# Performance work log

Measured on AMD Instinct MI355X. Metric: run time of the kernel, lower is better.

## Reference

```python
import jax, jax.numpy as jnp
import numpy as np

IMG = 800          # image size (square)
STRIDE = 4         # feature-map stride
S = 14             # rcnn_crop_size
C = 256            # crop_channels
N = 512            # number of rpn proposals
NUM_CLASSES = 81   # COCO (incl. background at index 0)
HID = 1024
NMS_TH = 0.5
SCORE_TH = 0.05


def setup_inputs() -> dict:
    key = jax.random.key(0)
    ks = jax.random.split(key, 8)
    features = jax.random.normal(ks[0], (1, C, IMG // STRIDE, IMG // STRIDE), jnp.float32)
    # valid proposal boxes (x0, y0, x1, y1) in image coordinates
    u = jax.random.uniform(ks[1], (N, 4), jnp.float32)
    x0 = u[:, 0] * (IMG - 64.0)
    y0 = u[:, 1] * (IMG - 64.0)
    bw = 16.0 + u[:, 2] * 240.0
    bh = 16.0 + u[:, 3] * 240.0
    proposals = jnp.stack([x0, y0, jnp.minimum(x0 + bw, IMG - 1.0), jnp.minimum(y0 + bh, IMG - 1.0)], axis=1)
    d1 = C * S * S  # 50176
    w1 = jax.random.normal(ks[2], (d1, HID), jnp.float32) * (1.0 / np.sqrt(d1))
    b1 = jnp.zeros((HID,), jnp.float32)
    w2 = jax.random.normal(ks[3], (HID, HID), jnp.float32) * (1.0 / np.sqrt(HID))
    b2 = jnp.zeros((HID,), jnp.float32)
    w_cls = jax.random.normal(ks[4], (HID, NUM_CLASSES), jnp.float32) * (1.0 / np.sqrt(HID))
    b_cls = jnp.zeros((NUM_CLASSES,), jnp.float32)
    w_reg = jax.random.normal(ks[5], (HID, NUM_CLASSES * 4), jnp.float32) * (1.0 / np.sqrt(HID))
    b_reg = jnp.zeros((NUM_CLASSES * 4,), jnp.float32)
    return dict(features=features, proposals=proposals, w1=w1, b1=b1, w2=w2, b2=b2,
                w_cls=w_cls, b_cls=b_cls, w_reg=w_reg, b_reg=b_reg)


def roi_align(feat, boxes):
    """feat: [C,H,W]; boxes: [N,4] image coords -> crops [N,C,S,S] via bilinear sampling (1 sample per bin)."""
    _, H, W = feat.shape
    b = boxes / STRIDE
    t = (jnp.arange(S, dtype=feat.dtype) + 0.5) / S                # [S] bin centers
    xs = b[:, 0:1] + (b[:, 2:3] - b[:, 0:1]) * t                   # [N,S]
    ys = b[:, 1:2] + (b[:, 3:4] - b[:, 1:2]) * t                   # [N,S]
    xx = jnp.broadcast_to(xs[:, None, :], (boxes.shape[0], S, S))  # [N,S,S]
    yy = jnp.broadcast_to(ys[:, :, None], (boxes.shape[0], S, S))
    x0f = jnp.floor(xx); y0f = jnp.floor(yy)
    fx = xx - x0f; fy = yy - y0f
    x0i = jnp.clip(x0f.astype(jnp.int32), 0, W - 1); x1i = jnp.clip(x0i + 1, 0, W - 1)
    y0i = jnp.clip(y0f.astype(jnp.int32), 0, H - 1); y1i = jnp.clip(y0i + 1, 0, H - 1)
    # gathers -> [C,N,S,S]
    v = (((1 - fx) * (1 - fy))[None] * feat[:, y0i, x0i]
         + (fx * (1 - fy))[None] * feat[:, y0i, x1i]
         + ((1 - fx) * fy)[None] * feat[:, y1i, x0i]
         + (fx * fy)[None] * feat[:, y1i, x1i])
    return v.transpose(1, 0, 2, 3)  # [N,C,S,S]


def decode_boxes(rois, d):
    w = rois[:, 2] - rois[:, 0]; h = rois[:, 3] - rois[:, 1]
    cx = rois[:, 0] + 0.5 * w; cy = rois[:, 1] + 0.5 * h
    px = cx + d[:, 0] * w; py = cy + d[:, 1] * h
    pw = w * jnp.exp(jnp.clip(d[:, 2], -4.0, 4.0))
    ph = h * jnp.exp(jnp.clip(d[:, 3], -4.0, 4.0))
    b = jnp.stack([px - 0.5 * pw, py - 0.5 * ph, px + 0.5 * pw, py + 0.5 * ph], axis=1)
    return jnp.clip(b, 0.0, IMG - 1.0)


def iou_matrix(b):
    area = jnp.maximum(b[:, 2] - b[:, 0], 0.0) * jnp.maximum(b[:, 3] - b[:, 1], 0.0)
    ix0 = jnp.maximum(b[:, None, 0], b[None, :, 0])
    iy0 = jnp.maximum(b[:, None, 1], b[None, :, 1])
    ix1 = jnp.minimum(b[:, None, 2], b[None, :, 2])
    iy1 = jnp.minimum(b[:, None, 3], b[None, :, 3])
    inter = jnp.maximum(ix1 - ix0, 0.0) * jnp.maximum(iy1 - iy0, 0.0)
    return inter / (area[:, None] + area[None, :] - inter + 1e-6)


def reference(features, proposals, w1, b1, w2, b2, w_cls, b_cls, w_reg, b_reg):
    # 1) RoIAlign crop
    crops = roi_align(features[0], proposals)              # [N,C,S,S]
    # 2) RCNN head
    x = crops.reshape(N, -1)
    x = jax.nn.relu(x @ w1 + b1)
    x = jax.nn.relu(x @ w2 + b2)
    logits = x @ w_cls + b_cls                             # [N,81]
    deltas = (x @ w_reg + b_reg).reshape(N, NUM_CLASSES, 4)
    # 3) NMS post-processing
    probs = jax.nn.softmax(logits, axis=-1)
    fg = probs[:, 1:]                                      # exclude background
    labels = jnp.argmax(fg, axis=-1) + 1                   # [N]
    scores = jnp.max(fg, axis=-1)                          # [N]
    d = deltas[jnp.arange(N), labels]                      # per-ROI delta of predicted class
    boxes = decode_boxes(proposals, d)
    order = jnp.argsort(-scores)
    bs = boxes[order]; ss = scores[order]; ls = labels[order]
    valid = ss > SCORE_TH
    M = iou_matrix(bs)                                     # [N,N]
    idx = jnp.arange(N)
    def body(i, keep):
        alive = keep[i] & valid[i]
        supp = (M[i] > NMS_TH) & (idx > i) & alive
        return keep & (~supp)
    keep = jax.lax.fori_loop(0, N, body, valid)
    keepf = jax.lax.stop_gradient(keep.astype(bs.dtype))
    final = jnp.concatenate([bs, ss[:, None]], axis=1) * keepf[:, None]   # [N,5]
    return final, ls.astype(jnp.int32), keep
```

## Files before the change

kernel.cpp:

```cpp
#include <hip/hip_runtime.h>
#include <cstdint>

#define F_H 200
#define F_W 200
#define D1  50176
#define NBOX 512
#define NHID 1024

typedef _Float16 f16;
typedef _Float16 half8 __attribute__((ext_vector_type(8)));
typedef float    f32x4 __attribute__((ext_vector_type(4)));

__device__ __forceinline__ void gload16(const void* g, void* l) {
  __builtin_amdgcn_global_load_lds((const __attribute__((address_space(1))) void*)g,
                                   (__attribute__((address_space(3))) void*)l,
                                   16, 0, 0);
}

__device__ __forceinline__ void splitf16(float v, f16& h, f16& l) {
  f16 hh = (f16)v;
  float hf = (float)hh;
  if (fabsf(hf) < 6.1035156e-5f) hf = 0.f;
  h = (f16)hf;
  l = (f16)((v - hf) * 2048.f);
}

__global__ __launch_bounds__(256) void k_roi(const float* __restrict__ feat,
                                             const float* __restrict__ prop,
                                             f16* __restrict__ xhi, f16* __restrict__ xlo) {
  uint32_t idx = blockIdx.x * 256u + threadIdx.x;
  uint32_t n = idx / D1;
  uint32_t rem = idx % D1;
  uint32_t c = rem / 196u;
  uint32_t r2 = rem % 196u;
  uint32_t i = r2 / 14u;
  uint32_t j = r2 % 14u;
  float b0 = prop[n * 4 + 0] * 0.25f, b1 = prop[n * 4 + 1] * 0.25f;
  float b2 = prop[n * 4 + 2] * 0.25f, b3 = prop[n * 4 + 3] * 0.25f;
  float tx = ((float)j + 0.5f) * (1.0f / 14.0f);
  float ty = ((float)i + 0.5f) * (1.0f / 14.0f);
  float xx = b0 + (b2 - b0) * tx;
  float yy = b1 + (b3 - b1) * ty;
  float x0f = floorf(xx), y0f = floorf(yy);
  float fx = xx - x0f, fy = yy - y0f;
  int x0 = (int)x0f; x0 = x0 < 0 ? 0 : (x0 > F_W - 1 ? F_W - 1 : x0);
  int y0 = (int)y0f; y0 = y0 < 0 ? 0 : (y0 > F_H - 1 ? F_H - 1 : y0);
  int x1 = x0 + 1 > F_W - 1 ? F_W - 1 : x0 + 1;
  int y1 = y0 + 1 > F_H - 1 ? F_H - 1 : y0 + 1;
  const float* fc = feat + (size_t)c * (F_H * F_W);
  float v00 = fc[y0 * F_W + x0], v01 = fc[y0 * F_W + x1];
  float v10 = fc[y1 * F_W + x0], v11 = fc[y1 * F_W + x1];
  float v = (1.f - fx) * (1.f - fy) * v00 + fx * (1.f - fy) * v01 +
            (1.f - fx) * fy * v10 + fx * fy * v11;
  f16 h, l; splitf16(v, h, l);
  xhi[idx] = h; xlo[idx] = l;
}

__global__ __launch_bounds__(256) void k_pack(const float* __restrict__ wc, const float* __restrict__ bc,
                                              const float* __restrict__ wr, const float* __restrict__ br,
                                              float* __restrict__ wh, float* __restrict__ bh) {
  uint32_t idx = blockIdx.x * 256u + threadIdx.x;
  if (idx < (uint32_t)NHID * 512u) {
    uint32_t k = idx >> 9, n = idx & 511u;
    float v = 0.f;
    if (n < 81u) v = wc[k * 81u + n];
    else if (n < 405u) v = wr[k * 324u + (n - 81u)];
    wh[idx] = v;
  } else if (idx < (uint32_t)NHID * 512u + 512u) {
    uint32_t n = idx - (uint32_t)NHID * 512u;
    float v = 0.f;
    if (n < 81u) v = bc[n];
    else if (n < 405u) v = br[n - 81u];
    bh[n] = v;
  }
}

__global__ __launch_bounds__(512, 2) void k_gemm(
    const f16* __restrict__ Ahi, const f16* __restrict__ Alo,
    const float* __restrict__ B, float* __restrict__ Cp,
    int K, int N, int Kc, int nMt, int nNt)
{
  __shared__ char sm[131072];
  const int t = threadIdx.x;
  const int lane = t & 63;
  const int wid = t >> 6;
  const int wr = wid >> 2;
  const int wc = wid & 3;
  const int rl = lane & 15;
  const int lq = lane >> 4;

  int bid = blockIdx.x;
  int low = bid & 7, q = bid >> 3;
  int nt = q % nNt;
  int chi = q / nNt;
  int c = chi * 8 + low;
  int ks = c / nMt;
  int mt = c % nMt;
  const int brow = mt * 256;
  const int nbase = nt * 256;
  const int k0 = ks * Kc;
  const int nk = Kc >> 5;

  uint32_t aoffg[2], aldso[2];
#pragma unroll
  for (int i = 0; i < 2; ++i) {
    uint32_t idx = (uint32_t)t + 512u * i;
    uint32_t r = idx >> 2, s = idx & 3;
    uint32_t sz = s ^ ((r >> 1) & 3);
    aoffg[i] = (uint32_t)(brow + r) * (uint32_t)K + sz * 8u;
    aldso[i] = idx * 16u;
  }
  uint32_t boffg[4], bldso[4];
#pragma unroll
  for (int i = 0; i < 4; ++i) {
    uint32_t idx = (uint32_t)t + 512u * i;
    uint32_t kr = idx >> 6, sg = idx & 63;
    boffg[i] = kr * (uint32_t)N + (uint32_t)nbase + sg * 4u;
    bldso[i] = idx * 16u;
  }

  const uint32_t a_off = (uint32_t)((wr * 128 + rl) * 64) + (uint32_t)((lq ^ ((rl >> 1) & 3)) * 16);
  const uint32_t b_off = 32768u + (uint32_t)(lq * 8192) + (uint32_t)((wc * 64 + rl) * 4);

  f32x4 zero4 = {0.f, 0.f, 0.f, 0.f};
  f32x4 acc[8][4];
#pragma unroll
  for (int m = 0; m < 8; ++m)
#pragma unroll
    for (int n = 0; n < 4; ++n) acc[m][n] = zero4;

  auto STAGE = [&](int buf, int kt) {
    uint32_t kb = (uint32_t)(k0 + kt * 32);
    char* lb = sm + buf * 65536;
#pragma unroll
    for (int i = 0; i < 2; ++i) {
      gload16(Ahi + aoffg[i] + kb, lb + aldso[i]);
      gload16(Alo + aoffg[i] + kb, lb + 16384 + aldso[i]);
    }
#pragma unroll
    for (int i = 0; i < 4; ++i) {
      gload16(B + (size_t)kb * (uint32_t)N + boffg[i], lb + 32768 + bldso[i]);
    }
  };

  STAGE(0, 0);
  __syncthreads();
  int cur = 0;
  for (int kt = 0; kt < nk; ++kt) {
    if (kt + 1 < nk) STAGE(cur ^ 1, kt + 1);
    const char* lb = sm + cur * 65536;

    half8 bh[4], bl[4];
#pragma unroll
    for (int nf = 0; nf < 4; ++nf) {
#pragma unroll
      for (int jj = 0; jj < 8; ++jj) {
        float v = *(const float*)(lb + b_off + nf * 64 + jj * 1024);
        f16 hh = (f16)v;
        float hf = (float)hh;
        if (fabsf(hf) < 6.1035156e-5f) hf = 0.f;
        bh[nf][jj] = (f16)hf;
        bl[nf][jj] = (f16)((v - hf) * 2048.f);
      }
    }
#pragma unroll
    for (int m = 0; m < 8; ++m) {
      half8 ah = *(const half8*)(lb + a_off + m * 1024);
      half8 al = *(const half8*)(lb + 16384 + a_off + m * 1024);
#pragma unroll
      for (int nf = 0; nf < 4; ++nf) {
        acc[m][nf] = __builtin_amdgcn_mfma_f32_16x16x32_f16(ah, bh[nf], acc[m][nf], 0, 0, 0);
        f32x4 tt = __builtin_amdgcn_mfma_f32_16x16x32_f16(ah, bl[nf], zero4, 0, 0, 0);
        tt = __builtin_amdgcn_mfma_f32_16x16x32_f16(al, bh[nf], tt, 0, 0, 0);
        acc[m][nf] += tt * 4.8828125e-4f;
      }
    }
    __syncthreads();
    cur ^= 1;
  }

  float* Cs = Cp + (size_t)ks * ((size_t)512 * (uint32_t)N);
#pragma unroll
  for (int m = 0; m < 8; ++m) {
    int rg = brow + wr * 128 + m * 16 + lq * 4;
#pragma unroll
    for (int nf = 0; nf < 4; ++nf) {
      int cg = nbase + wc * 64 + nf * 16 + rl;
#pragma unroll
      for (int rr = 0; rr < 4; ++rr)
        Cs[(size_t)(rg + rr) * (uint32_t)N + cg] = acc[m][nf][rr];
    }
  }
}

__global__ __launch_bounds__(256) void k_reduce(
    const float* __restrict__ parts, const float* __restrict__ bias,
    int nS, int MN, int Ncols, int relu,
    float* __restrict__ outf, f16* __restrict__ ohi, f16* __restrict__ olo)
{
  uint32_t idx = blockIdx.x * 256u + threadIdx.x;
  if (idx >= (uint32_t)MN) return;
  float s = bias[idx % (uint32_t)Ncols];
  for (int i = 0; i < nS; ++i) s += parts[(size_t)i * (uint32_t)MN + idx];
  if (relu) s = fmaxf(s, 0.f);
  if (outf) outf[idx] = s;
  if (ohi) { f16 h, l; splitf16(s, h, l); ohi[idx] = h; olo[idx] = l; }
}

__global__ __launch_bounds__(256) void k_post(
    const float* __restrict__ ld, const float* __restrict__ prop,
    float* __restrict__ boxes, float* __restrict__ scores, int* __restrict__ labels)
{
  int n = blockIdx.x * 256 + threadIdx.x;
  if (n >= NBOX) return;
  const float* L = ld + (size_t)n * 512;
  float m = L[0];
  for (int j = 1; j < 81; ++j) m = fmaxf(m, L[j]);
  float sum = 0.f;
  for (int j = 0; j < 81; ++j) sum += expf(L[j] - m);
  float best = -1.f; int bj = 1;
  for (int j = 1; j < 81; ++j) {
    float p = expf(L[j] - m) / sum;
    if (p > best) { best = p; bj = j; }
  }
  float d0 = L[81 + bj * 4 + 0];
  float d1 = L[81 + bj * 4 + 1];
  float d2 = L[81 + bj * 4 + 2];
  float d3 = L[81 + bj * 4 + 3];
  float p0 = prop[n * 4 + 0], p1 = prop[n * 4 + 1], p2 = prop[n * 4 + 2], p3 = prop[n * 4 + 3];
  float w = p2 - p0, h = p3 - p1;
  float cx = p0 + 0.5f * w, cy = p1 + 0.5f * h;
  float px = cx + d0 * w, py = cy + d1 * h;
  float pw = w * expf(fminf(fmaxf(d2, -4.f), 4.f));
  float ph = h * expf(fminf(fmaxf(d3, -4.f), 4.f));
  float bx0 = px - 0.5f * pw, by0 = py - 0.5f * ph;
  float bx1 = px + 0.5f * pw, by1 = py + 0.5f * ph;
  boxes[n * 4 + 0] = fminf(fmaxf(bx0, 0.f), 799.f);
  boxes[n * 4 + 1] = fminf(fmaxf(by0, 0.f), 799.f);
  boxes[n * 4 + 2] = fminf(fmaxf(bx1, 0.f), 799.f);
  boxes[n * 4 + 3] = fminf(fmaxf(by1, 0.f), 799.f);
  scores[n] = best;
  labels[n] = bj;
}

__global__ __launch_bounds__(512) void k_sort(
    const float* __restrict__ scores, const float* __restrict__ boxes, const int* __restrict__ labels,
    float* __restrict__ bs, float* __restrict__ ss, int* __restrict__ ls)
{
  __shared__ unsigned long long keys[512];
  int t = threadIdx.x;
  unsigned sb = __float_as_uint(scores[t]);
  keys[t] = ((unsigned long long)(0xFFFFFFFFu - sb) << 32) | (unsigned)t;
  __syncthreads();
  for (int k = 2; k <= 512; k <<= 1) {
    for (int j = k >> 1; j > 0; j >>= 1) {
      int p = t ^ j;
      if (p > t) {
        unsigned long long a = keys[t], b = keys[p];
        bool asc = ((t & k) == 0);
        if (asc ? (a > b) : (a < b)) { keys[t] = b; keys[p] = a; }
      }
      __syncthreads();
    }
  }
  unsigned o = (unsigned)(keys[t] & 0xFFFFFFFFu);
  ss[t] = scores[o];
  ls[t] = labels[o];
  bs[t * 4 + 0] = boxes[o * 4 + 0];
  bs[t * 4 + 1] = boxes[o * 4 + 1];
  bs[t * 4 + 2] = boxes[o * 4 + 2];
  bs[t * 4 + 3] = boxes[o * 4 + 3];
}

__global__ __launch_bounds__(64) void k_mask(const float* __restrict__ bs,
                                             unsigned long long* __restrict__ mask) {
  int i = blockIdx.x;
  int lane = threadIdx.x;
  float ax0 = bs[i * 4], ay0 = bs[i * 4 + 1], ax1 = bs[i * 4 + 2], ay1 = bs[i * 4 + 3];
  float aarea = fmaxf(ax1 - ax0, 0.f) * fmaxf(ay1 - ay0, 0.f);
  for (int w = 0; w < 8; ++w) {
    int j = w * 64 + lane;
    float bx0 = bs[j * 4], by0 = bs[j * 4 + 1], bx1 = bs[j * 4 + 2], by1 = bs[j * 4 + 3];
    float barea = fmaxf(bx1 - bx0, 0.f) * fmaxf(by1 - by0, 0.f);
    float ix0 = fmaxf(ax0, bx0), iy0 = fmaxf(ay0, by0);
    float ix1 = fminf(ax1, bx1), iy1 = fminf(ay1, by1);
    float inter = fmaxf(ix1 - ix0, 0.f) * fmaxf(iy1 - iy0, 0.f);
    float iou = inter / (aarea + barea - inter + 1e-6f);
    bool cond = (iou > 0.5f) && (j > i);
    unsigned long long b = __ballot(cond);
    if (lane == 0) mask[i * 8 + w] = b;
  }
}

__global__ __launch_bounds__(64) void k_nms(const unsigned long long* __restrict__ mask,
                                            const float* __restrict__ ss,
                                            const float* __restrict__ bs,
                                            const int* __restrict__ ls,
                                            float* __restrict__ out) {
  int lane = threadIdx.x;
  unsigned long long bal[8];
  for (int w = 0; w < 8; ++w) bal[w] = __ballot(ss[w * 64 + lane] > 0.05f);
  unsigned long long keep = (lane < 8) ? bal[lane] : 0ULL;
  for (int i = 0; i < 512; ++i) {
    unsigned long long kw = __shfl(keep, i >> 6);
    if ((kw >> (i & 63)) & 1ULL) {
      unsigned long long mi = (lane < 8) ? mask[i * 8 + lane] : 0ULL;
      keep &= ~mi;
    }
  }
  __shared__ unsigned long long kws[8];
  if (lane < 8) kws[lane] = keep;
  __syncthreads();
  for (int it = 0; it < 56; ++it) {
    int idx = lane + it * 64;
    float val;
    if (idx < 2560) {
      int i = idx / 5, c2 = idx % 5;
      bool kb = (kws[i >> 6] >> (i & 63)) & 1ULL;
      val = kb ? (c2 < 4 ? bs[i * 4 + c2] : ss[i]) : 0.f;
    } else if (idx < 3072) {
      int i = idx - 2560;
      val = (float)ls[i];
    } else {
      int i = idx - 3072;
      val = ((kws[i >> 6] >> (i & 63)) & 1ULL) ? 1.f : 0.f;
    }
    out[idx] = val;
  }
}

static constexpr size_t SZ_X    = (size_t)NBOX * D1 * 2;
static constexpr size_t OFF_XHI = 0;
static constexpr size_t OFF_XLO = OFF_XHI + SZ_X;
static constexpr size_t OFF_PART = OFF_XLO + SZ_X;
static constexpr size_t SZ_PART = (size_t)32 * 512 * 1024 * 4;
static constexpr size_t SZ_H    = (size_t)512 * 1024 * 2;
static constexpr size_t OFF_H1HI = OFF_PART + SZ_PART;
static constexpr size_t OFF_H1LO = OFF_H1HI + SZ_H;
static constexpr size_t OFF_H2HI = OFF_H1LO + SZ_H;
static constexpr size_t OFF_H2LO = OFF_H2HI + SZ_H;
static constexpr size_t OFF_WH   = OFF_H2LO + SZ_H;
static constexpr size_t OFF_BH   = OFF_WH + (size_t)1024 * 512 * 4;
static constexpr size_t OFF_LD   = OFF_BH + 4096;
static constexpr size_t OFF_BOX  = OFF_LD + (size_t)512 * 512 * 4;
static constexpr size_t OFF_SC   = OFF_BOX + 512 * 4 * 4;
static constexpr size_t OFF_LB   = OFF_SC + 4096;
static constexpr size_t OFF_BS   = OFF_LB + 4096;
static constexpr size_t OFF_SS   = OFF_BS + 512 * 4 * 4;
static constexpr size_t OFF_LS   = OFF_SS + 4096;
static constexpr size_t OFF_MASK = OFF_LS + 4096;
static constexpr size_t OFF_END  = OFF_MASK + (size_t)512 * 8 * 8;

extern "C" void kernel_launch(void* const* d_in, const int* in_sizes, int n_in,
                              void* d_out, int out_size, void* d_ws, size_t ws_size,
                              hipStream_t stream)
{
  (void)in_sizes; (void)n_in;
  const float* feat = (const float*)d_in[0];
  const float* prop = (const float*)d_in[1];
  const float* w1   = (const float*)d_in[2];
  const float* b1   = (const float*)d_in[3];
  const float* w2   = (const float*)d_in[4];
  const float* b2   = (const float*)d_in[5];
  const float* wcls = (const float*)d_in[6];
  const float* bcls = (const float*)d_in[7];
  const float* wreg = (const float*)d_in[8];
  const float* breg = (const float*)d_in[9];
  float* out = (float*)d_out;
  char* W = (char*)d_ws;

  if (ws_size < OFF_END) {
    hipMemsetAsync(out, 0x7f, (size_t)out_size * 4, stream);
    return;
  }

  f16*   xhi   = (f16*)(W + OFF_XHI);
  f16*   xlo   = (f16*)(W + OFF_XLO);
  float* parts = (float*)(W + OFF_PART);
  f16*   h1hi  = (f16*)(W + OFF_H1HI);
  f16*   h1lo  = (f16*)(W + OFF_H1LO);
  f16*   h2hi  = (f16*)(W + OFF_H2HI);
  f16*   h2lo  = (f16*)(W + OFF_H2LO);
  float* whead = (float*)(W + OFF_WH);
  float* bhead = (float*)(W + OFF_BH);
  float* ldbuf = (float*)(W + OFF_LD);
  float* boxes = (float*)(W + OFF_BOX);
  float* scores= (float*)(W + OFF_SC);
  int*   labels= (int*)(W + OFF_LB);
  float* bsrt  = (float*)(W + OFF_BS);
  float* ssrt  = (float*)(W + OFF_SS);
  int*   lsrt  = (int*)(W + OFF_LS);
  unsigned long long* maskb = (unsigned long long*)(W + OFF_MASK);

  k_pack<<<2050, 256, 0, stream>>>(wcls, bcls, wreg, breg, whead, bhead);
  k_roi<<<(NBOX * D1) / 256, 256, 0, stream>>>(feat, prop, xhi, xlo);

  k_gemm<<<256, 512, 0, stream>>>(xhi, xlo, w1, parts, D1, 1024, 1568, 2, 4);
  k_reduce<<<2048, 256, 0, stream>>>(parts, b1, 32, 512 * 1024, 1024, 1, nullptr, h1hi, h1lo);

  k_gemm<<<64, 512, 0, stream>>>(h1hi, h1lo, w2, parts, 1024, 1024, 128, 2, 4);
  k_reduce<<<2048, 256, 0, stream>>>(parts, b2, 8, 512 * 1024, 1024, 1, nullptr, h2hi, h2lo);

  k_gemm<<<64, 512, 0, stream>>>(h2hi, h2lo, whead, parts, 1024, 512, 64, 2, 2);
  k_reduce<<<1024, 256, 0, stream>>>(parts, bhead, 16, 512 * 512, 512, 0, ldbuf, nullptr, nullptr);

  k_post<<<2, 256, 0, stream>>>(ldbuf, prop, boxes, scores, labels);
  k_sort<<<1, 512, 0, stream>>>(scores, boxes, labels, bsrt, ssrt, lsrt);
  k_mask<<<512, 64, 0, stream>>>(bsrt, maskb);
  k_nms<<<1, 64, 0, stream>>>(maskb, ssrt, bsrt, lsrt, out);
}
```

Measured before the change: 436.2 us.

## Split GEMM k-loop into two phases, swizzle B tiles, vectorize ROI and reduce

The GEMM main loop is restructured into two half-phases. Each phase issues part of the next stage's global-to-LDS loads, with explicit vmcnt waits and barriers in place of a full __syncthreads, so loads overlap MFMA work. B tiles are XOR-swizzled in LDS to cut bank conflicts, and the fp32-to-f16 hi/lo split now uses packed cvt_pkrtz with MFMA priority hints. The ROI kernel produces two output elements per thread and the reduce kernel works on float4 vectors. The hand-tuned waitcnt/barrier scheduling is fragile, and round-toward-zero conversion changes rounding of the split.

```diff
diff --git a/kernel.cpp b/kernel.cpp
--- a/kernel.cpp
+++ b/kernel.cpp
@@ -9,12 +9,18 @@
 
 typedef _Float16 f16;
 typedef _Float16 half8 __attribute__((ext_vector_type(8)));
+typedef _Float16 half4v __attribute__((ext_vector_type(4)));
+typedef _Float16 half2v __attribute__((ext_vector_type(2)));
 typedef float    f32x4 __attribute__((ext_vector_type(4)));
 
 __device__ __forceinline__ void gload16(const void* g, void* l) {
   __builtin_amdgcn_global_load_lds((const __attribute__((address_space(1))) void*)g,
                                    (__attribute__((address_space(3))) void*)l,
                                    16, 0, 0);
+}
+
+__device__ __forceinline__ half2v pkrtz(float a, float b) {
+  return __builtin_bit_cast(half2v, __builtin_amdgcn_cvt_pkrtz(a, b));
 }
 
 __device__ __forceinline__ void splitf16(float v, f16& h, f16& l) {
@@ -29,31 +35,42 @@
                                              const float* __restrict__ prop,
                                              f16* __restrict__ xhi, f16* __restrict__ xlo) {
   uint32_t idx = blockIdx.x * 256u + threadIdx.x;
-  uint32_t n = idx / D1;
-  uint32_t rem = idx % D1;
-  uint32_t c = rem / 196u;
-  uint32_t r2 = rem % 196u;
-  uint32_t i = r2 / 14u;
-  uint32_t j = r2 % 14u;
+  uint32_t n = idx / 25088u;
+  uint32_t rem = idx % 25088u;
+  uint32_t c = rem / 98u;
+  uint32_t r2 = rem % 98u;
+  uint32_t i = r2 / 7u;
+  uint32_t jp = r2 % 7u;
   float b0 = prop[n * 4 + 0] * 0.25f, b1 = prop[n * 4 + 1] * 0.25f;
   float b2 = prop[n * 4 + 2] * 0.25f, b3 = prop[n * 4 + 3] * 0.25f;
-  float tx = ((float)j + 0.5f) * (1.0f / 14.0f);
   float ty = ((float)i + 0.5f) * (1.0f / 14.0f);
-  float xx = b0 + (b2 - b0) * tx;
   float yy = b1 + (b3 - b1) * ty;
-  float x0f = floorf(xx), y0f = floorf(yy);
-  float fx = xx - x0f, fy = yy - y0f;
-  int x0 = (int)x0f; x0 = x0 < 0 ? 0 : (x0 > F_W - 1 ? F_W - 1 : x0);
+  float y0f = floorf(yy);
+  float fy = yy - y0f;
   int y0 = (int)y0f; y0 = y0 < 0 ? 0 : (y0 > F_H - 1 ? F_H - 1 : y0);
-  int x1 = x0 + 1 > F_W - 1 ? F_W - 1 : x0 + 1;
   int y1 = y0 + 1 > F_H - 1 ? F_H - 1 : y0 + 1;
-  const float* fc = feat + (size_t)c * (F_H * F_W);
-  float v00 = fc[y0 * F_W + x0], v01 = fc[y0 * F_W + x1];
-  float v10 = fc[y1 * F_W + x0], v11 = fc[y1 * F_W + x1];
-  float v = (1.f - fx) * (1.f - fy) * v00 + fx * (1.f - fy) * v01 +
-            (1.f - fx) * fy * v10 + fx * fy * v11;
-  f16 h, l; splitf16(v, h, l);
-  xhi[idx] = h; xlo[idx] = l;
+  const float* fr0 = feat + (size_t)c * (F_H * F_W) + (size_t)y0 * F_W;
+  const float* fr1 = feat + (size_t)c * (F_H * F_W) + (size_t)y1 * F_W;
+  f16 hs[2], ls[2];
+#pragma unroll
+  for (int e = 0; e < 2; ++e) {
+    uint32_t j = jp * 2u + (uint32_t)e;
+    float tx = ((float)j + 0.5f) * (1.0f / 14.0f);
+    float xx = b0 + (b2 - b0) * tx;
+    float x0f = floorf(xx);
+    float fx = xx - x0f;
+    int x0 = (int)x0f; x0 = x0 < 0 ? 0 : (x0 > F_W - 1 ? F_W - 1 : x0);
+    int x1 = x0 + 1 > F_W - 1 ? F_W - 1 : x0 + 1;
+    float v00 = fr0[x0], v01 = fr0[x1], v10 = fr1[x0], v11 = fr1[x1];
+    float v = (1.f - fx) * (1.f - fy) * v00 + fx * (1.f - fy) * v01 +
+              (1.f - fx) * fy * v10 + fx * fy * v11;
+    splitf16(v, hs[e], ls[e]);
+  }
+  uint32_t base = n * 50176u + c * 196u + i * 14u + jp * 2u;
+  half2v hv; hv[0] = hs[0]; hv[1] = hs[1];
+  half2v lv; lv[0] = ls[0]; lv[1] = ls[1];
+  *(half2v*)(xhi + base) = hv;
+  *(half2v*)(xlo + base) = lv;
 }
 
 __global__ __launch_bounds__(256) void k_pack(const float* __restrict__ wc, const float* __restrict__ bc,
@@ -110,17 +127,20 @@
     aoffg[i] = (uint32_t)(brow + r) * (uint32_t)K + sz * 8u;
     aldso[i] = idx * 16u;
   }
-  uint32_t boffg[4], bldso[4];
-#pragma unroll
-  for (int i = 0; i < 4; ++i) {
-    uint32_t idx = (uint32_t)t + 512u * i;
-    uint32_t kr = idx >> 6, sg = idx & 63;
-    boffg[i] = kr * (uint32_t)N + (uint32_t)nbase + sg * 4u;
-    bldso[i] = idx * 16u;
-  }
-
-  const uint32_t a_off = (uint32_t)((wr * 128 + rl) * 64) + (uint32_t)((lq ^ ((rl >> 1) & 3)) * 16);
-  const uint32_t b_off = 32768u + (uint32_t)(lq * 8192) + (uint32_t)((wc * 64 + rl) * 4);
+  uint32_t boffg[2][2], bldso[2][2];
+#pragma unroll
+  for (int h = 0; h < 2; ++h)
+#pragma unroll
+    for (int i = 0; i < 2; ++i) {
+      uint32_t idx = (uint32_t)t + 512u * i;
+      uint32_t kr = idx >> 5, sg = idx & 31;
+      uint32_t sgs = sg ^ (((kr >> 3) & 3) << 2);
+      boffg[h][i] = kr * (uint32_t)N + (uint32_t)(nbase + h * 128) + sgs * 4u;
+      bldso[h][i] = 32768u + (uint32_t)h * 16384u + idx * 16u;
+    }
+
+  const uint32_t a_off = (uint32_t)(wr * 8192 + rl * 64) + (uint32_t)((lq ^ ((rl >> 1) & 3)) * 16);
+  const uint32_t b_lane = (uint32_t)((((wc ^ lq) & 3) * 16 + rl) * 4);
 
   f32x4 zero4 = {0.f, 0.f, 0.f, 0.f};
   f32x4 acc[8][4];
@@ -129,53 +149,77 @@
 #pragma unroll
     for (int n = 0; n < 4; ++n) acc[m][n] = zero4;
 
-  auto STAGE = [&](int buf, int kt) {
-    uint32_t kb = (uint32_t)(k0 + kt * 32);
-    char* lb = sm + buf * 65536;
-#pragma unroll
-    for (int i = 0; i < 2; ++i) {
-      gload16(Ahi + aoffg[i] + kb, lb + aldso[i]);
-      gload16(Alo + aoffg[i] + kb, lb + 16384 + aldso[i]);
-    }
-#pragma unroll
-    for (int i = 0; i < 4; ++i) {
-      gload16(B + (size_t)kb * (uint32_t)N + boffg[i], lb + 32768 + bldso[i]);
-    }
-  };
-
-  STAGE(0, 0);
-  __syncthreads();
+#define STAGE_A(LB, KB) do { \
+    gload16(Ahi + aoffg[0] + (KB), (LB) + aldso[0]); \
+    gload16(Alo + aoffg[0] + (KB), (LB) + 16384 + aldso[0]); \
+    gload16(Ahi + aoffg[1] + (KB), (LB) + aldso[1]); \
+    gload16(Alo + aoffg[1] + (KB), (LB) + 16384 + aldso[1]); \
+  } while (0)
+
+#define STAGE_B(LB, KB) do { \
+    gload16(B + (size_t)(KB) * (uint32_t)N + boffg[0][0], (LB) + bldso[0][0]); \
+    gload16(B + (size_t)(KB) * (uint32_t)N + boffg[0][1], (LB) + bldso[0][1]); \
+    gload16(B + (size_t)(KB) * (uint32_t)N + boffg[1][0], (LB) + bldso[1][0]); \
+    gload16(B + (size_t)(KB) * (uint32_t)N + boffg[1][1], (LB) + bldso[1][1]); \
+  } while (0)
+
+#define COMPUTE_PHASE(P) do { \
+    half8 bhv[2], blv[2]; \
+    _Pragma("unroll") \
+    for (int x = 0; x < 2; ++x) { \
+      const int nf = 2 * (P) + x; \
+      const char* bb = lb + 32768 + (nf >> 1) * 16384 + (nf & 1) * 256 + b_lane; \
+      _Pragma("unroll") \
+      for (int jj = 0; jj < 8; jj += 2) { \
+        float v0 = *(const float*)(bb + (lq * 8 + jj) * 512); \
+        float v1 = *(const float*)(bb + (lq * 8 + jj + 1) * 512); \
+        half2v hp = pkrtz(v0, v1); \
+        f16 e0 = (fabsf(v0) >= 6.1035156e-5f) ? hp[0] : (f16)0; \
+        f16 e1 = (fabsf(v1) >= 6.1035156e-5f) ? hp[1] : (f16)0; \
+        half2v lp = pkrtz((v0 - (float)e0) * 2048.f, (v1 - (float)e1) * 2048.f); \
+        bhv[x][jj] = e0; bhv[x][jj + 1] = e1; \
+        blv[x][jj] = lp[0]; blv[x][jj + 1] = lp[1]; \
+      } \
+    } \
+    __builtin_amdgcn_s_setprio(1); \
+    _Pragma("unroll") \
+    for (int m = 0; m < 8; ++m) { \
+      half8 ah = *(const half8*)(lb + a_off + m * 1024); \
+      half8 al = *(const half8*)(lb + 16384 + a_off + m * 1024); \
+      _Pragma("unroll") \
+      for (int x = 0; x < 2; ++x) { \
+        const int nf = 2 * (P) + x; \
+        acc[m][nf] = __builtin_amdgcn_mfma_f32_16x16x32_f16(ah, bhv[x], acc[m][nf], 0, 0, 0); \
+        f32x4 tt = __builtin_amdgcn_mfma_f32_16x16x32_f16(ah, blv[x], zero4, 0, 0, 0); \
+        tt = __builtin_amdgcn_mfma_f32_16x16x32_f16(al, bhv[x], tt, 0, 0, 0); \
+        acc[m][nf] += tt * 4.8828125e-4f; \
+      } \
+    } \
+    __builtin_amdgcn_s_setprio(0); \
+  } while (0)
+
+  STAGE_A(sm, (uint32_t)k0);
+  STAGE_B(sm, (uint32_t)k0);
+
   int cur = 0;
   for (int kt = 0; kt < nk; ++kt) {
-    if (kt + 1 < nk) STAGE(cur ^ 1, kt + 1);
+    int ktn = (kt + 1 < nk) ? kt + 1 : kt;
+    uint32_t kbn = (uint32_t)(k0 + ktn * 32);
     const char* lb = sm + cur * 65536;
-
-    half8 bh[4], bl[4];
-#pragma unroll
-    for (int nf = 0; nf < 4; ++nf) {
-#pragma unroll
-      for (int jj = 0; jj < 8; ++jj) {
-        float v = *(const float*)(lb + b_off + nf * 64 + jj * 1024);
-        f16 hh = (f16)v;
-        float hf = (float)hh;
-        if (fabsf(hf) < 6.1035156e-5f) hf = 0.f;
-        bh[nf][jj] = (f16)hf;
-        bl[nf][jj] = (f16)((v - hf) * 2048.f);
-      }
-    }
-#pragma unroll
-    for (int m = 0; m < 8; ++m) {
-      half8 ah = *(const half8*)(lb + a_off + m * 1024);
-      half8 al = *(const half8*)(lb + 16384 + a_off + m * 1024);
-#pragma unroll
-      for (int nf = 0; nf < 4; ++nf) {
-        acc[m][nf] = __builtin_amdgcn_mfma_f32_16x16x32_f16(ah, bh[nf], acc[m][nf], 0, 0, 0);
-        f32x4 tt = __builtin_amdgcn_mfma_f32_16x16x32_f16(ah, bl[nf], zero4, 0, 0, 0);
-        tt = __builtin_amdgcn_mfma_f32_16x16x32_f16(al, bh[nf], tt, 0, 0, 0);
-        acc[m][nf] += tt * 4.8828125e-4f;
-      }
-    }
-    __syncthreads();
+    char* lbn = sm + (cur ^ 1) * 65536;
+
+    asm volatile("s_waitcnt vmcnt(2)" ::: "memory");
+    __builtin_amdgcn_s_barrier();
+    __builtin_amdgcn_sched_barrier(0);
+    STAGE_A(lbn, kbn);
+    COMPUTE_PHASE(0);
+
+    asm volatile("s_waitcnt vmcnt(4)" ::: "memory");
+    __builtin_amdgcn_s_barrier();
+    __builtin_amdgcn_sched_barrier(0);
+    STAGE_B(lbn, kbn);
+    COMPUTE_PHASE(1);
+
     cur ^= 1;
   }
 
@@ -185,26 +229,39 @@
     int rg = brow + wr * 128 + m * 16 + lq * 4;
 #pragma unroll
     for (int nf = 0; nf < 4; ++nf) {
-      int cg = nbase + wc * 64 + nf * 16 + rl;
+      int cg = nbase + nf * 64 + wc * 16 + rl;
 #pragma unroll
       for (int rr = 0; rr < 4; ++rr)
         Cs[(size_t)(rg + rr) * (uint32_t)N + cg] = acc[m][nf][rr];
     }
   }
+#undef STAGE_A
+#undef STAGE_B
+#undef COMPUTE_PHASE
 }
 
 __global__ __launch_bounds__(256) void k_reduce(
     const float* __restrict__ parts, const float* __restrict__ bias,
-    int nS, int MN, int Ncols, int relu,
+    int nS, int MN4, int Ncols, int relu,
     float* __restrict__ outf, f16* __restrict__ ohi, f16* __restrict__ olo)
 {
   uint32_t idx = blockIdx.x * 256u + threadIdx.x;
-  if (idx >= (uint32_t)MN) return;
-  float s = bias[idx % (uint32_t)Ncols];
-  for (int i = 0; i < nS; ++i) s += parts[(size_t)i * (uint32_t)MN + idx];
-  if (relu) s = fmaxf(s, 0.f);
-  if (outf) outf[idx] = s;
-  if (ohi) { f16 h, l; splitf16(s, h, l); ohi[idx] = h; olo[idx] = l; }
+  if (idx >= (uint32_t)MN4) return;
+  f32x4 s = *(const f32x4*)(bias + ((idx * 4u) % (uint32_t)Ncols));
+  const f32x4* p4 = (const f32x4*)parts;
+  for (int i = 0; i < nS; ++i) s += p4[(size_t)i * (uint32_t)MN4 + idx];
+  if (relu) {
+#pragma unroll
+    for (int j = 0; j < 4; ++j) s[j] = fmaxf(s[j], 0.f);
+  }
+  if (outf) *(f32x4*)(outf + (size_t)idx * 4) = s;
+  if (ohi) {
+    half4v h, l;
+#pragma unroll
+    for (int j = 0; j < 4; ++j) { f16 hh, ll; splitf16(s[j], hh, ll); h[j] = hh; l[j] = ll; }
+    *(half4v*)(ohi + (size_t)idx * 4) = h;
+    *(half4v*)(olo + (size_t)idx * 4) = l;
+  }
 }
 
 __global__ __launch_bounds__(256) void k_post(
@@ -370,7 +427,7 @@
   char* W = (char*)d_ws;
 
   if (ws_size < OFF_END) {
-    hipMemsetAsync(out, 0x7f, (size_t)out_size * 4, stream);
+    (void)hipMemsetAsync(out, 0x7f, (size_t)out_size * 4, stream);
     return;
   }
 
@@ -393,16 +450,16 @@
   unsigned long long* maskb = (unsigned long long*)(W + OFF_MASK);
 
   k_pack<<<2050, 256, 0, stream>>>(wcls, bcls, wreg, breg, whead, bhead);
-  k_roi<<<(NBOX * D1) / 256, 256, 0, stream>>>(feat, prop, xhi, xlo);
+  k_roi<<<50176, 256, 0, stream>>>(feat, prop, xhi, xlo);
 
   k_gemm<<<256, 512, 0, stream>>>(xhi, xlo, w1, parts, D1, 1024, 1568, 2, 4);
-  k_reduce<<<2048, 256, 0, stream>>>(parts, b1, 32, 512 * 1024, 1024, 1, nullptr, h1hi, h1lo);
+  k_reduce<<<512, 256, 0, stream>>>(parts, b1, 32, 131072, 1024, 1, nullptr, h1hi, h1lo);
 
   k_gemm<<<64, 512, 0, stream>>>(h1hi, h1lo, w2, parts, 1024, 1024, 128, 2, 4);
-  k_reduce<<<2048, 256, 0, stream>>>(parts, b2, 8, 512 * 1024, 1024, 1, nullptr, h2hi, h2lo);
+  k_reduce<<<512, 256, 0, stream>>>(parts, b2, 8, 131072, 1024, 1, nullptr, h2hi, h2lo);
 
   k_gemm<<<64, 512, 0, stream>>>(h2hi, h2lo, whead, parts, 1024, 512, 64, 2, 2);
-  k_reduce<<<1024, 256, 0, stream>>>(parts, bhead, 16, 512 * 512, 512, 0, ldbuf, nullptr, nullptr);
+  k_reduce<<<256, 256, 0, stream>>>(parts, bhead, 16, 65536, 512, 0, ldbuf, nullptr, nullptr);
 
   k_post<<<2, 256, 0, stream>>>(ldbuf, prop, boxes, scores, labels);
   k_sort<<<1, 512, 0, stream>>>(scores, boxes, labels, bsrt, ssrt, lsrt);
```

Measured after the change: 415.8 us. 1.05x faster.
